# Optimization experiments

Measured on AMD Instinct MI355X. Metric: run time of the kernel, lower is better.

## Reference

```python
import jax, jax.numpy as jnp
import numpy as np

S, B, E, H, DFF = 1024, 4, 1024, 16, 4096
D = E // H  # head_dim = 64
EPS = 1e-5


def setup_inputs() -> dict:
    key = jax.random.key(0)
    ks = jax.random.split(key, 16)
    rn = lambda k, shape, s: jax.random.normal(k, shape, jnp.float32) * s
    # RoPE tables (half-rotation), theta=10000
    inv_freq = 1.0 / (10000.0 ** (jnp.arange(0, D, 2, dtype=jnp.float32) / D))  # [D/2]
    ang = jnp.arange(S, dtype=jnp.float32)[:, None] * inv_freq[None, :]          # [S, D/2]
    return {
        "q": rn(ks[0], (S, B, E), 1.0),
        "in_proj_w": rn(ks[1], (3 * E, E), E ** -0.5),
        "in_proj_b": rn(ks[2], (3 * E,), 0.02),
        "out_w": rn(ks[3], (E, E), E ** -0.5),
        "out_b": rn(ks[4], (E,), 0.02),
        "ln1_g": jnp.ones((E,), jnp.float32) + rn(ks[5], (E,), 0.02),
        "ln1_b": rn(ks[6], (E,), 0.02),
        "ln2_g": jnp.ones((E,), jnp.float32) + rn(ks[7], (E,), 0.02),
        "ln2_b": rn(ks[8], (E,), 0.02),
        "ff1_w": rn(ks[9], (DFF, E), E ** -0.5),
        "ff1_b": rn(ks[10], (DFF,), 0.02),
        "ff2_w": rn(ks[11], (E, DFF), DFF ** -0.5),
        "ff2_b": rn(ks[12], (E,), 0.02),
        "rope_cos": jnp.cos(ang),
        "rope_sin": jnp.sin(ang),
    }


def _layernorm(x, g, b):
    mu = jnp.mean(x, -1, keepdims=True)
    var = jnp.mean((x - mu) ** 2, -1, keepdims=True)
    return (x - mu) * jax.lax.rsqrt(var + EPS) * g + b


def reference(q, in_proj_w, in_proj_b, out_w, out_b, ln1_g, ln1_b, ln2_g, ln2_b,
              ff1_w, ff1_b, ff2_w, ff2_b, rope_cos, rope_sin):
    s, b, e = q.shape
    d = 2 * rope_cos.shape[-1]
    h = e // d
    # pre-norm (self-attention: k = v = q, so norm computed once)
    xq = _layernorm(q, ln1_g, ln1_b)
    # fused QKV projection
    qkv = xq @ in_proj_w.T + in_proj_b            # [s, b, 3e]
    qh, kh, vh = jnp.split(qkv, 3, axis=-1)
    qh = qh.reshape(s, b, h, d)
    kh = kh.reshape(s, b, h, d)
    vh = vh.reshape(s, b, h, d)

    def rope(t):
        t1, t2 = jnp.split(t, 2, axis=-1)          # [s, b, h, d/2] each
        c = rope_cos[:, None, None, :]
        sn = rope_sin[:, None, None, :]
        return jnp.concatenate([t1 * c - t2 * sn, t1 * sn + t2 * c], axis=-1)

    qh = rope(qh)
    kh = rope(kh)
    # attention (ssmax='none' -> identity scaling, dropout=0, no masks)
    scores = jnp.einsum("sbhd,tbhd->bhst", qh, kh) / jnp.sqrt(jnp.float32(d))
    attn = jax.nn.softmax(scores, axis=-1)
    ao = jnp.einsum("bhst,tbhd->sbhd", attn, vh).reshape(s, b, e)
    ao = ao @ out_w.T + out_b
    # residual + pre-norm FFN
    x = q + ao
    y = _layernorm(x, ln2_g, ln2_b)
    ff = jax.nn.gelu(y @ ff1_w.T + ff1_b, approximate=False) @ ff2_w.T + ff2_b
    return x + ff
```

## Files before the change

kernel.cpp:

```cpp
#include <hip/hip_runtime.h>
#include <hip/hip_bf16.h>
#include <stdint.h>

typedef float f32x4 __attribute__((ext_vector_type(4)));
typedef __bf16 bf16x8 __attribute__((ext_vector_type(8)));

__device__ __forceinline__ unsigned short f2bf(float f) {
    union { float f; unsigned u; } v; v.f = f;
    unsigned r = v.u + 0x7fffu + ((v.u >> 16) & 1u);
    return (unsigned short)(r >> 16);
}
__device__ __forceinline__ float bf2f(unsigned short u) {
    union { unsigned u; float f; } v; v.u = ((unsigned)u) << 16;
    return v.f;
}
__device__ __forceinline__ unsigned cvt_pk_bf16(float lo, float hi) {
    unsigned r;
    asm("v_cvt_pk_bf16_f32 %0, %1, %2" : "=v"(r) : "v"(lo), "v"(hi));
    return r;
}

__device__ __forceinline__ void gl_lds16(const void* g, void* l) {
    __builtin_amdgcn_global_load_lds(
        (const __attribute__((address_space(1))) void*)(unsigned long long)(uintptr_t)g,
        (__attribute__((address_space(3))) void*)(unsigned)(uintptr_t)l,
        16, 0, 0);
}

__global__ __launch_bounds__(256) void cvt_kernel(const float* __restrict__ in,
                                                  unsigned short* __restrict__ outp) {
    int i = blockIdx.x * 256 + threadIdx.x;
    float4 v = ((const float4*)in)[i];
    ushort4 o;
    o.x = f2bf(v.x); o.y = f2bf(v.y); o.z = f2bf(v.z); o.w = f2bf(v.w);
    ((ushort4*)outp)[i] = o;
}

__global__ __launch_bounds__(256) void ln_kernel(const float* __restrict__ x,
                                                 const float* __restrict__ g,
                                                 const float* __restrict__ b,
                                                 unsigned short* __restrict__ outp) {
    const int row = blockIdx.x;
    const int t = threadIdx.x;
    const float4 v = ((const float4*)(x + (size_t)row * 1024))[t];
    float s = v.x + v.y + v.z + v.w;
    float s2 = v.x * v.x + v.y * v.y + v.z * v.z + v.w * v.w;
    #pragma unroll
    for (int off = 1; off < 64; off <<= 1) {
        s  += __shfl_xor(s, off);
        s2 += __shfl_xor(s2, off);
    }
    __shared__ float red[8];
    const int w = t >> 6;
    if ((t & 63) == 0) { red[w * 2] = s; red[w * 2 + 1] = s2; }
    __syncthreads();
    s  = red[0] + red[2] + red[4] + red[6];
    s2 = red[1] + red[3] + red[5] + red[7];
    const float mu = s * (1.0f / 1024.0f);
    const float var = s2 * (1.0f / 1024.0f) - mu * mu;
    const float rstd = rsqrtf(var + 1e-5f);
    const float4 gv = ((const float4*)g)[t];
    const float4 bv = ((const float4*)b)[t];
    ushort4 o;
    o.x = f2bf((v.x - mu) * rstd * gv.x + bv.x);
    o.y = f2bf((v.y - mu) * rstd * gv.y + bv.y);
    o.z = f2bf((v.z - mu) * rstd * gv.z + bv.z);
    o.w = f2bf((v.w - mu) * rstd * gv.w + bv.w);
    ((ushort4*)(outp + (size_t)row * 1024))[t] = o;
}

__global__ __launch_bounds__(512) void rope_kernel(const unsigned short* __restrict__ qkv,
                                                   const float* __restrict__ rc,
                                                   const float* __restrict__ rs,
                                                   unsigned short* __restrict__ Qr,
                                                   unsigned short* __restrict__ Kr) {
    const int sb = blockIdx.x;
    const int s = sb >> 2, b = sb & 3;
    const int t = threadIdx.x;
    const int h = t >> 5, d = t & 31;
    const size_t rowo = (size_t)sb * 3072;
    const float c = rc[s * 32 + d];
    const float sn = rs[s * 32 + d];
    const size_t ho = ((size_t)(b * 16 + h) * 1024 + s) * 64;

    const float q1 = bf2f(qkv[rowo + h * 64 + d]);
    const float q2 = bf2f(qkv[rowo + h * 64 + d + 32]);
    Qr[ho + d]      = f2bf((q1 * c - q2 * sn) * 0.125f);
    Qr[ho + d + 32] = f2bf((q1 * sn + q2 * c) * 0.125f);

    const float k1 = bf2f(qkv[rowo + 1024 + h * 64 + d]);
    const float k2 = bf2f(qkv[rowo + 1024 + h * 64 + d + 32]);
    Kr[ho + d]      = f2bf(k1 * c - k2 * sn);
    Kr[ho + d + 32] = f2bf(k1 * sn + k2 * c);
}

__global__ __launch_bounds__(256) void vt_kernel(const unsigned short* __restrict__ qkv,
                                                 unsigned short* __restrict__ Vt) {
    __shared__ unsigned short t[64][66];
    const int s0 = blockIdx.x * 64;
    const int bh = blockIdx.y;
    const int b = bh >> 4, h = bh & 15;
    const int tid = threadIdx.x;
    const int si = tid >> 3, c = (tid & 7) * 8;
    #pragma unroll
    for (int r = 0; r < 2; r++) {
        const int s = si + r * 32;
        union { uint4 u; unsigned short sh[8]; } v;
        v.u = *(const uint4*)&qkv[((size_t)(s0 + s) * 4 + b) * 3072 + 2048 + h * 64 + c];
        #pragma unroll
        for (int i = 0; i < 8; i++) t[c + i][s] = v.sh[i];
    }
    __syncthreads();
    #pragma unroll
    for (int r = 0; r < 2; r++) {
        const int d = si + r * 32;
        const unsigned* rp = (const unsigned*)((const char*)&t[0][0] + d * 132 + c * 2);
        uint4 ov;
        ov.x = rp[0]; ov.y = rp[1]; ov.z = rp[2]; ov.w = rp[3];
        *(uint4*)&Vt[((size_t)bh * 64 + d) * 1024 + s0 + c] = ov;
    }
}

template <int EPI>
__global__ __launch_bounds__(512, 4)
void gemmW(const unsigned short* __restrict__ A, const unsigned short* __restrict__ Bw,
           const float* __restrict__ bias, unsigned short* __restrict__ Cout,
           int N, int K, int nbx) {
    __shared__ __attribute__((aligned(16))) unsigned short smem[32768];
    unsigned short* As = smem;
    unsigned short* Bs = smem + 16384;

    const int nwg = gridDim.x;
    const int swz = (blockIdx.x & 7) * (nwg >> 3) + (blockIdx.x >> 3);
    const int by = swz / nbx, bx = swz % nbx;
    const int bm = by * 256, bn = bx * 128;

    const int tid = threadIdx.x;
    const int w = tid >> 6, l = tid & 63;
    const int wr = w >> 2, wc = w & 3;
    const int lm = l & 15, lg = l >> 4, lx = lm & 7;

    const int srow = tid >> 3;
    const int sgx = ((tid & 7) ^ (srow & 7)) * 8;
    const int sdst = (tid & 7) * 8;
    const unsigned short* Ag = A + (size_t)(bm + srow) * K + sgx;
    const unsigned short* Bg = Bw + (size_t)(bn + srow) * K + sgx;

    const int c0 = ((lg ^ lx) << 3);
    const int c1 = (((4 + lg) ^ lx) << 3);

    f32x4 acc[8][2];
    #pragma unroll
    for (int i = 0; i < 8; i++)
        #pragma unroll
        for (int j = 0; j < 2; j++) acc[i][j] = f32x4{0.f, 0.f, 0.f, 0.f};

    const int arow = wr * 128 + lm;
    const int brow = wc * 32 + lm;

    for (int k0 = 0; k0 < K; k0 += 64) {
        __syncthreads();
        #pragma unroll
        for (int i = 0; i < 4; i++)
            gl_lds16(Ag + (size_t)(i * 64) * K + k0, &As[(srow + i * 64) * 64 + sdst]);
        #pragma unroll
        for (int i = 0; i < 2; i++)
            gl_lds16(Bg + (size_t)(i * 64) * K + k0, &Bs[(srow + i * 64) * 64 + sdst]);
        __syncthreads();
        #pragma unroll
        for (int h = 0; h < 2; h++) {
            const int cc = h ? c1 : c0;
            bf16x8 af[8], bfr[2];
            #pragma unroll
            for (int ni = 0; ni < 2; ni++)
                bfr[ni] = *(const bf16x8*)&Bs[(brow + ni * 16) * 64 + cc];
            #pragma unroll
            for (int mi = 0; mi < 8; mi++)
                af[mi] = *(const bf16x8*)&As[(arow + mi * 16) * 64 + cc];
            #pragma unroll
            for (int mi = 0; mi < 8; mi++)
                #pragma unroll
                for (int ni = 0; ni < 2; ni++)
                    acc[mi][ni] = __builtin_amdgcn_mfma_f32_16x16x32_bf16(
                        af[mi], bfr[ni], acc[mi][ni], 0, 0, 0);
        }
    }

    __syncthreads();
    const int r0l = wr * 128 + lg * 4;
    #pragma unroll
    for (int ni = 0; ni < 2; ni++) {
        const int col = wc * 32 + ni * 16 + lm;
        const float bc = bias[bn + col];
        #pragma unroll
        for (int mi = 0; mi < 8; mi++) {
            #pragma unroll
            for (int j = 0; j < 4; j++) {
                const int row = r0l + mi * 16 + j;
                float v = acc[mi][ni][j] + bc;
                if constexpr (EPI == 2)
                    v = 0.5f * v * (1.0f + erff(v * 0.70710678118654752f));
                smem[row * 128 + col] = f2bf(v);
            }
        }
    }
    __syncthreads();
    const int orow = tid >> 4, oseg = (tid & 15) * 8;
    #pragma unroll
    for (int p = 0; p < 8; p++) {
        const int row = p * 32 + orow;
        const uint4 v = *(const uint4*)&smem[row * 128 + oseg];
        *(uint4*)&Cout[(size_t)(bm + row) * N + bn + oseg] = v;
    }
}

template <int EPI, int BM, int BN, int WM, int WN, bool CM>
__global__ __launch_bounds__((BM / WM) * (BN / WN) * 64, 2)
void gemm4(const unsigned short* __restrict__ A, const unsigned short* __restrict__ Bw,
           const float* __restrict__ bias, const float* __restrict__ res,
           void* __restrict__ Cout, int N, int K, int nbx) {
    constexpr int WAVES_N = BN / WN;
    constexpr int THREADS = (BM / WM) * (BN / WN) * 64;
    constexpr int MR = WM / 16, NR = WN / 16;
    constexpr int ASZ = BM * 64, BSZ = BN * 64;
    constexpr int RPP = THREADS / 8;
    static_assert(BM / RPP + BN / RPP == 8, "STAGE must issue exactly 8 loads");
    __shared__ __attribute__((aligned(16))) unsigned short As[2 * ASZ];
    __shared__ __attribute__((aligned(16))) unsigned short Bs[2 * BSZ];

    const int nwg = gridDim.x;
    const int swz = (blockIdx.x & 7) * (nwg >> 3) + (blockIdx.x >> 3);
    const int nby = nwg / nbx;
    const int bx = CM ? (swz / nby) : (swz % nbx);
    const int by = CM ? (swz % nby) : (swz / nbx);
    const int bm = by * BM, bn = bx * BN;

    const int tid = threadIdx.x;
    const int w = tid >> 6, l = tid & 63;
    const int wr = w / WAVES_N, wc = w % WAVES_N;
    const int lm = l & 15, lg = l >> 4, lx = lm & 7;

    const int srow = tid >> 3;
    const int sgx = ((tid & 7) ^ (srow & 7)) * 8;
    const unsigned short* Ag = A + (size_t)(bm + srow) * K + sgx;
    const unsigned short* Bg = Bw + (size_t)(bn + srow) * K + sgx;

    const int c0 = ((lg ^ lx) << 3);
    const int c1 = (((4 + lg) ^ lx) << 3);

    f32x4 acc[MR][NR];
    #pragma unroll
    for (int i = 0; i < MR; i++)
        #pragma unroll
        for (int j = 0; j < NR; j++) acc[i][j] = f32x4{0.f, 0.f, 0.f, 0.f};

    auto STAGE = [&](int buf, int k0) {
        #pragma unroll
        for (int i = 0; i < BM / RPP; i++)
            gl_lds16(Ag + (size_t)i * RPP * K + k0, &As[buf * ASZ + i * RPP * 64 + tid * 8]);
        #pragma unroll
        for (int i = 0; i < BN / RPP; i++)
            gl_lds16(Bg + (size_t)i * RPP * K + k0, &Bs[buf * BSZ + i * RPP * 64 + tid * 8]);
    };

    const int NT = K >> 6;
    STAGE(0, 0);
    STAGE(1, 64);

    int cur = 0;
    for (int t = 0; t < NT; ++t) {
        if (t + 1 < NT) asm volatile("s_waitcnt vmcnt(8)" ::: "memory");
        else            asm volatile("s_waitcnt vmcnt(0)" ::: "memory");
        __builtin_amdgcn_s_barrier();
        asm volatile("" ::: "memory");

        const int ab = cur * ASZ, bb = cur * BSZ;
        #pragma unroll
        for (int h = 0; h < 2; h++) {
            const int cc = h ? c1 : c0;
            bf16x8 af[MR], bfr[NR];
            #pragma unroll
            for (int mi = 0; mi < MR; mi++)
                af[mi] = *(const bf16x8*)&As[ab + (wr * WM + mi * 16 + lm) * 64 + cc];
            #pragma unroll
            for (int ni = 0; ni < NR; ni++)
                bfr[ni] = *(const bf16x8*)&Bs[bb + (wc * WN + ni * 16 + lm) * 64 + cc];
            __builtin_amdgcn_s_setprio(1);
            #pragma unroll
            for (int mi = 0; mi < MR; mi++)
                #pragma unroll
                for (int ni = 0; ni < NR; ni++)
                    acc[mi][ni] = __builtin_amdgcn_mfma_f32_16x16x32_bf16(
                        af[mi], bfr[ni], acc[mi][ni], 0, 0, 0);
            __builtin_amdgcn_s_setprio(0);
        }

        asm volatile("" ::: "memory");
        __builtin_amdgcn_s_barrier();
        asm volatile("" ::: "memory");
        if (t + 2 < NT) STAGE(cur, (t + 2) << 6);
        cur ^= 1;
    }

    const int r0 = bm + wr * WM + lg * 4;
    #pragma unroll
    for (int ni = 0; ni < NR; ni++) {
        const int col = bn + wc * WN + ni * 16 + lm;
        const float bc = bias[col];
        #pragma unroll
        for (int mi = 0; mi < MR; mi++) {
            #pragma unroll
            for (int j = 0; j < 4; j++) {
                const int row = r0 + mi * 16 + j;
                const size_t idx = (size_t)row * N + col;
                const float v = acc[mi][ni][j] + bc;
                if constexpr (EPI == 0) {
                    ((unsigned short*)Cout)[idx] = f2bf(v);
                } else if constexpr (EPI == 1) {
                    ((float*)Cout)[idx] = v + res[idx];
                } else if constexpr (EPI == 2) {
                    const float ge = 0.5f * v * (1.0f + erff(v * 0.70710678118654752f));
                    ((unsigned short*)Cout)[idx] = f2bf(ge);
                } else {
                    ((float*)Cout)[idx] = v + res[idx];
                }
            }
        }
    }
}

__global__ __launch_bounds__(256, 4)
void attn_kernel(const unsigned short* __restrict__ Qr, const unsigned short* __restrict__ Kr,
                 const unsigned short* __restrict__ Vt, unsigned short* __restrict__ AO) {
    __shared__ __attribute__((aligned(16))) unsigned short Ks[64][72];
    __shared__ __attribute__((aligned(16))) unsigned short Vs[64][72];
    const int tid = threadIdx.x;
    const int w = tid >> 6, l = tid & 63;
    const int lm = l & 15, lg = l >> 4;
    const int qt = blockIdx.x, bh = blockIdx.y;
    const size_t hoff = (size_t)bh * (1024 * 64);

    const size_t qrow = hoff + (size_t)(qt * 64 + w * 16 + lm) * 64;
    const bf16x8 qf0 = *(const bf16x8*)&Qr[qrow + lg * 8];
    const bf16x8 qf1 = *(const bf16x8*)&Qr[qrow + 32 + lg * 8];

    float m = -1e30f, lsum = 0.f;
    f32x4 acc[4];
    #pragma unroll
    for (int i = 0; i < 4; i++) acc[i] = f32x4{0.f, 0.f, 0.f, 0.f};

    const int sr = tid >> 3, scc = (tid & 7) * 8;
    const int srcA = lm + 16 * ((2 * lg) & 3);
    const int srcB = lm + 16 * ((2 * lg + 1) & 3);
    const bool hi2 = (lg & 2) != 0;

    uint4 kr0 = *(const uint4*)&Kr[hoff + (size_t)sr * 64 + scc];
    uint4 kr1 = *(const uint4*)&Kr[hoff + (size_t)(sr + 32) * 64 + scc];
    uint4 vr0 = *(const uint4*)&Vt[hoff + (size_t)sr * 1024 + scc];
    uint4 vr1 = *(const uint4*)&Vt[hoff + (size_t)(sr + 32) * 1024 + scc];

    for (int kt = 0; kt < 16; kt++) {
        __syncthreads();
        *(uint4*)&Ks[sr][scc]      = kr0;
        *(uint4*)&Ks[sr + 32][scc] = kr1;
        *(uint4*)&Vs[sr][scc]      = vr0;
        *(uint4*)&Vs[sr + 32][scc] = vr1;
        __syncthreads();
        if (kt < 15) {
            const size_t kb = hoff + (size_t)(kt + 1) * 64 * 64;
            kr0 = *(const uint4*)&Kr[kb + (size_t)sr * 64 + scc];
            kr1 = *(const uint4*)&Kr[kb + (size_t)(sr + 32) * 64 + scc];
            vr0 = *(const uint4*)&Vt[hoff + (size_t)sr * 1024 + (kt + 1) * 64 + scc];
            vr1 = *(const uint4*)&Vt[hoff + (size_t)(sr + 32) * 1024 + (kt + 1) * 64 + scc];
        }

        f32x4 st[4];
        #pragma unroll
        for (int nt = 0; nt < 4; nt++) {
            const bf16x8 kf0 = *(const bf16x8*)&Ks[nt * 16 + lm][lg * 8];
            const bf16x8 kf1 = *(const bf16x8*)&Ks[nt * 16 + lm][32 + lg * 8];
            f32x4 s = f32x4{0.f, 0.f, 0.f, 0.f};
            s = __builtin_amdgcn_mfma_f32_16x16x32_bf16(kf0, qf0, s, 0, 0, 0);
            s = __builtin_amdgcn_mfma_f32_16x16x32_bf16(kf1, qf1, s, 0, 0, 0);
            st[nt] = s;
        }

        float tmax = st[0][0];
        #pragma unroll
        for (int nt = 0; nt < 4; nt++)
            #pragma unroll
            for (int j = 0; j < 4; j++) tmax = fmaxf(tmax, st[nt][j]);
        tmax = fmaxf(tmax, __shfl_xor(tmax, 16));
        tmax = fmaxf(tmax, __shfl_xor(tmax, 32));

        const float mnew = fmaxf(m, tmax);
        const float fac = __builtin_amdgcn_exp2f((m - mnew) * 1.4426950408889634f);
        m = mnew;

        unsigned pd[4][2];
        float rsum = 0.f;
        #pragma unroll
        for (int nt = 0; nt < 4; nt++) {
            const float p0 = __builtin_amdgcn_exp2f((st[nt][0] - mnew) * 1.4426950408889634f);
            const float p1 = __builtin_amdgcn_exp2f((st[nt][1] - mnew) * 1.4426950408889634f);
            const float p2 = __builtin_amdgcn_exp2f((st[nt][2] - mnew) * 1.4426950408889634f);
            const float p3 = __builtin_amdgcn_exp2f((st[nt][3] - mnew) * 1.4426950408889634f);
            rsum += (p0 + p1) + (p2 + p3);
            pd[nt][0] = cvt_pk_bf16(p0, p1);
            pd[nt][1] = cvt_pk_bf16(p2, p3);
        }
        rsum += __shfl_xor(rsum, 16);
        rsum += __shfl_xor(rsum, 32);
        lsum = lsum * fac + rsum;
        #pragma unroll
        for (int nt2 = 0; nt2 < 4; nt2++)
            #pragma unroll
            for (int j = 0; j < 4; j++) acc[nt2][j] *= fac;

        #pragma unroll
        for (int kt2 = 0; kt2 < 2; kt2++) {
            const int a0 = __shfl((int)pd[kt2 * 2][0], srcA);
            const int a1 = __shfl((int)pd[kt2 * 2 + 1][0], srcA);
            const int a2 = __shfl((int)pd[kt2 * 2][1], srcA);
            const int a3 = __shfl((int)pd[kt2 * 2 + 1][1], srcA);
            const int b0 = __shfl((int)pd[kt2 * 2][0], srcB);
            const int b1 = __shfl((int)pd[kt2 * 2 + 1][0], srcB);
            const int b2 = __shfl((int)pd[kt2 * 2][1], srcB);
            const int b3 = __shfl((int)pd[kt2 * 2 + 1][1], srcB);
            union { int u[4]; bf16x8 v; } pf;
            pf.u[0] = hi2 ? a1 : a0;
            pf.u[1] = hi2 ? a3 : a2;
            pf.u[2] = hi2 ? b1 : b0;
            pf.u[3] = hi2 ? b3 : b2;
            #pragma unroll
            for (int nt2 = 0; nt2 < 4; nt2++) {
                const bf16x8 vf = *(const bf16x8*)&Vs[nt2 * 16 + lm][kt2 * 32 + lg * 8];
                acc[nt2] = __builtin_amdgcn_mfma_f32_16x16x32_bf16(vf, pf.v, acc[nt2], 0, 0, 0);
            }
        }
    }

    const int b = bh >> 4, h = bh & 15;
    const float inv = 1.0f / lsum;
    const int s = qt * 64 + w * 16 + lm;
    #pragma unroll
    for (int nt2 = 0; nt2 < 4; nt2++) {
        ushort4 o;
        o.x = f2bf(acc[nt2][0] * inv);
        o.y = f2bf(acc[nt2][1] * inv);
        o.z = f2bf(acc[nt2][2] * inv);
        o.w = f2bf(acc[nt2][3] * inv);
        *(ushort4*)&AO[(size_t)(s * 4 + b) * 1024 + h * 64 + nt2 * 16 + lg * 4] = o;
    }
}

extern "C" void kernel_launch(void* const* d_in, const int* in_sizes, int n_in,
                              void* d_out, int out_size, void* d_ws, size_t ws_size,
                              hipStream_t stream) {
    const float* q    = (const float*)d_in[0];
    const float* w_in = (const float*)d_in[1];
    const float* b_in = (const float*)d_in[2];
    const float* w_o  = (const float*)d_in[3];
    const float* b_o  = (const float*)d_in[4];
    const float* g1   = (const float*)d_in[5];
    const float* be1  = (const float*)d_in[6];
    const float* g2   = (const float*)d_in[7];
    const float* be2  = (const float*)d_in[8];
    const float* w1   = (const float*)d_in[9];
    const float* b1   = (const float*)d_in[10];
    const float* w2   = (const float*)d_in[11];
    const float* b2   = (const float*)d_in[12];
    const float* rc   = (const float*)d_in[13];
    const float* rsn  = (const float*)d_in[14];
    float* outp = (float*)d_out;

    char* base = (char*)d_ws;
    if (ws_size < 109051904ull) return;

    unsigned short* wb_in  = (unsigned short*)(base + 0);
    unsigned short* wb_out = wb_in + 3145728;
    unsigned short* wb_ff1 = wb_out + 1048576;
    unsigned short* wb_ff2 = wb_ff1 + 4194304;
    unsigned short* xq  = (unsigned short*)(base + 25165824);
    unsigned short* qkv = (unsigned short*)(base + 33554432);
    unsigned short* hh  = (unsigned short*)(base + 33554432);
    unsigned short* Qr  = (unsigned short*)(base + 58720256);
    unsigned short* Kr  = (unsigned short*)(base + 67108864);
    unsigned short* Vt  = (unsigned short*)(base + 75497472);
    unsigned short* ao  = (unsigned short*)(base + 83886080);
    float*          x   = (float*)(base + 92274688);
    unsigned short* y   = xq;

    cvt_kernel<<<3072, 256, 0, stream>>>(w_in, wb_in);
    cvt_kernel<<<1024, 256, 0, stream>>>(w_o, wb_out);
    cvt_kernel<<<4096, 256, 0, stream>>>(w1, wb_ff1);
    cvt_kernel<<<4096, 256, 0, stream>>>(w2, wb_ff2);

    ln_kernel<<<4096, 256, 0, stream>>>(q, g1, be1, xq);
    gemmW<0><<<384, 512, 0, stream>>>(xq, wb_in, b_in, qkv, 3072, 1024, 24);
    rope_kernel<<<4096, 512, 0, stream>>>(qkv, rc, rsn, Qr, Kr);
    vt_kernel<<<dim3(16, 64), 256, 0, stream>>>(qkv, Vt);
    attn_kernel<<<dim3(16, 64), 256, 0, stream>>>(Qr, Kr, Vt, ao);
    gemm4<1, 128, 128, 64, 64, true><<<256, 256, 0, stream>>>(ao, wb_out, b_o, q, x, 1024, 1024, 8);
    ln_kernel<<<4096, 256, 0, stream>>>(x, g2, be2, y);
    gemmW<2><<<512, 512, 0, stream>>>(y, wb_ff1, b1, hh, 4096, 1024, 32);
    gemm4<3, 128, 128, 64, 64, true><<<256, 256, 0, stream>>>(hh, wb_ff2, b2, x, outp, 1024, 4096, 8);
}
```

Measured before the change: 226.5 us.

## Group GEMM tile rasterization for L2 reuse and widen attention KV tiles

Adds a grouped tile-mapping helper so consecutive workgroups on each XCD cover a compact GR×GC block of output tiles. This improves L2 reuse of the A and B panels in the QKV, out-proj and FFN GEMMs, and gemm4 is specialised to a fixed 128x128 shape. The attention kernel now processes 128 keys per iteration instead of 64, halving the loop trips and barriers. The cost is more registers for scores and prefetch buffers, plus larger LDS, which may reduce occupancy.

```diff
diff --git a/kernel.cpp b/kernel.cpp
--- a/kernel.cpp
+++ b/kernel.cpp
@@ -25,6 +25,16 @@
         (const __attribute__((address_space(1))) void*)(unsigned long long)(uintptr_t)g,
         (__attribute__((address_space(3))) void*)(unsigned)(uintptr_t)l,
         16, 0, 0);
+}
+
+__device__ __forceinline__ void tile_map(int bid, int nwg, int nbx, int GR, int GC,
+                                         int* bx, int* by) {
+    const int swz = (bid & 7) * (nwg >> 3) + (bid >> 3);
+    const int CH = nwg >> 3;
+    const int chunk = swz / CH, ii = swz % CH;
+    const int KC = nbx / GC;
+    *bx = (chunk % KC) * GC + (ii % GC);
+    *by = (chunk / KC) * GR + (ii / GC);
 }
 
 __global__ __launch_bounds__(256) void cvt_kernel(const float* __restrict__ in,
@@ -121,7 +131,7 @@
     }
 }
 
-template <int EPI>
+template <int EPI, int GR, int GC>
 __global__ __launch_bounds__(512, 4)
 void gemmW(const unsigned short* __restrict__ A, const unsigned short* __restrict__ Bw,
            const float* __restrict__ bias, unsigned short* __restrict__ Cout,
@@ -130,9 +140,8 @@
     unsigned short* As = smem;
     unsigned short* Bs = smem + 16384;
 
-    const int nwg = gridDim.x;
-    const int swz = (blockIdx.x & 7) * (nwg >> 3) + (blockIdx.x >> 3);
-    const int by = swz / nbx, bx = swz % nbx;
+    int bx, by;
+    tile_map(blockIdx.x, gridDim.x, nbx, GR, GC, &bx, &by);
     const int bm = by * 256, bn = bx * 128;
 
     const int tid = threadIdx.x;
@@ -214,30 +223,22 @@
     }
 }
 
-template <int EPI, int BM, int BN, int WM, int WN, bool CM>
-__global__ __launch_bounds__((BM / WM) * (BN / WN) * 64, 2)
+template <int EPI, int GR, int GC>
+__global__ __launch_bounds__(256, 2)
 void gemm4(const unsigned short* __restrict__ A, const unsigned short* __restrict__ Bw,
            const float* __restrict__ bias, const float* __restrict__ res,
            void* __restrict__ Cout, int N, int K, int nbx) {
-    constexpr int WAVES_N = BN / WN;
-    constexpr int THREADS = (BM / WM) * (BN / WN) * 64;
-    constexpr int MR = WM / 16, NR = WN / 16;
-    constexpr int ASZ = BM * 64, BSZ = BN * 64;
-    constexpr int RPP = THREADS / 8;
-    static_assert(BM / RPP + BN / RPP == 8, "STAGE must issue exactly 8 loads");
+    constexpr int ASZ = 128 * 64, BSZ = 128 * 64;
     __shared__ __attribute__((aligned(16))) unsigned short As[2 * ASZ];
     __shared__ __attribute__((aligned(16))) unsigned short Bs[2 * BSZ];
 
-    const int nwg = gridDim.x;
-    const int swz = (blockIdx.x & 7) * (nwg >> 3) + (blockIdx.x >> 3);
-    const int nby = nwg / nbx;
-    const int bx = CM ? (swz / nby) : (swz % nbx);
-    const int by = CM ? (swz % nby) : (swz / nbx);
-    const int bm = by * BM, bn = bx * BN;
+    int bx, by;
+    tile_map(blockIdx.x, gridDim.x, nbx, GR, GC, &bx, &by);
+    const int bm = by * 128, bn = bx * 128;
 
     const int tid = threadIdx.x;
     const int w = tid >> 6, l = tid & 63;
-    const int wr = w / WAVES_N, wc = w % WAVES_N;
+    const int wr = w >> 1, wc = w & 1;
     const int lm = l & 15, lg = l >> 4, lx = lm & 7;
 
     const int srow = tid >> 3;
@@ -248,19 +249,19 @@
     const int c0 = ((lg ^ lx) << 3);
     const int c1 = (((4 + lg) ^ lx) << 3);
 
-    f32x4 acc[MR][NR];
-    #pragma unroll
-    for (int i = 0; i < MR; i++)
-        #pragma unroll
-        for (int j = 0; j < NR; j++) acc[i][j] = f32x4{0.f, 0.f, 0.f, 0.f};
+    f32x4 acc[4][4];
+    #pragma unroll
+    for (int i = 0; i < 4; i++)
+        #pragma unroll
+        for (int j = 0; j < 4; j++) acc[i][j] = f32x4{0.f, 0.f, 0.f, 0.f};
 
     auto STAGE = [&](int buf, int k0) {
         #pragma unroll
-        for (int i = 0; i < BM / RPP; i++)
-            gl_lds16(Ag + (size_t)i * RPP * K + k0, &As[buf * ASZ + i * RPP * 64 + tid * 8]);
-        #pragma unroll
-        for (int i = 0; i < BN / RPP; i++)
-            gl_lds16(Bg + (size_t)i * RPP * K + k0, &Bs[buf * BSZ + i * RPP * 64 + tid * 8]);
+        for (int i = 0; i < 4; i++)
+            gl_lds16(Ag + (size_t)i * 32 * K + k0, &As[buf * ASZ + i * 32 * 64 + tid * 8]);
+        #pragma unroll
+        for (int i = 0; i < 4; i++)
+            gl_lds16(Bg + (size_t)i * 32 * K + k0, &Bs[buf * BSZ + i * 32 * 64 + tid * 8]);
     };
 
     const int NT = K >> 6;
@@ -278,18 +279,18 @@
         #pragma unroll
         for (int h = 0; h < 2; h++) {
             const int cc = h ? c1 : c0;
-            bf16x8 af[MR], bfr[NR];
-            #pragma unroll
-            for (int mi = 0; mi < MR; mi++)
-                af[mi] = *(const bf16x8*)&As[ab + (wr * WM + mi * 16 + lm) * 64 + cc];
-            #pragma unroll
-            for (int ni = 0; ni < NR; ni++)
-                bfr[ni] = *(const bf16x8*)&Bs[bb + (wc * WN + ni * 16 + lm) * 64 + cc];
+            bf16x8 af[4], bfr[4];
+            #pragma unroll
+            for (int mi = 0; mi < 4; mi++)
+                af[mi] = *(const bf16x8*)&As[ab + (wr * 64 + mi * 16 + lm) * 64 + cc];
+            #pragma unroll
+            for (int ni = 0; ni < 4; ni++)
+                bfr[ni] = *(const bf16x8*)&Bs[bb + (wc * 64 + ni * 16 + lm) * 64 + cc];
             __builtin_amdgcn_s_setprio(1);
             #pragma unroll
-            for (int mi = 0; mi < MR; mi++)
+            for (int mi = 0; mi < 4; mi++)
                 #pragma unroll
-                for (int ni = 0; ni < NR; ni++)
+                for (int ni = 0; ni < 4; ni++)
                     acc[mi][ni] = __builtin_amdgcn_mfma_f32_16x16x32_bf16(
                         af[mi], bfr[ni], acc[mi][ni], 0, 0, 0);
             __builtin_amdgcn_s_setprio(0);
@@ -302,13 +303,13 @@
         cur ^= 1;
     }
 
-    const int r0 = bm + wr * WM + lg * 4;
-    #pragma unroll
-    for (int ni = 0; ni < NR; ni++) {
-        const int col = bn + wc * WN + ni * 16 + lm;
+    const int r0 = bm + wr * 64 + lg * 4;
+    #pragma unroll
+    for (int ni = 0; ni < 4; ni++) {
+        const int col = bn + wc * 64 + ni * 16 + lm;
         const float bc = bias[col];
         #pragma unroll
-        for (int mi = 0; mi < MR; mi++) {
+        for (int mi = 0; mi < 4; mi++) {
             #pragma unroll
             for (int j = 0; j < 4; j++) {
                 const int row = r0 + mi * 16 + j;
@@ -316,8 +317,6 @@
                 const float v = acc[mi][ni][j] + bc;
                 if constexpr (EPI == 0) {
                     ((unsigned short*)Cout)[idx] = f2bf(v);
-                } else if constexpr (EPI == 1) {
-                    ((float*)Cout)[idx] = v + res[idx];
                 } else if constexpr (EPI == 2) {
                     const float ge = 0.5f * v * (1.0f + erff(v * 0.70710678118654752f));
                     ((unsigned short*)Cout)[idx] = f2bf(ge);
@@ -332,8 +331,8 @@
 __global__ __launch_bounds__(256, 4)
 void attn_kernel(const unsigned short* __restrict__ Qr, const unsigned short* __restrict__ Kr,
                  const unsigned short* __restrict__ Vt, unsigned short* __restrict__ AO) {
-    __shared__ __attribute__((aligned(16))) unsigned short Ks[64][72];
-    __shared__ __attribute__((aligned(16))) unsigned short Vs[64][72];
+    __shared__ __attribute__((aligned(16))) unsigned short Ks[128][72];
+    __shared__ __attribute__((aligned(16))) unsigned short Vs[64][136];
     const int tid = threadIdx.x;
     const int w = tid >> 6, l = tid & 63;
     const int lm = l & 15, lg = l >> 4;
@@ -349,34 +348,39 @@
     #pragma unroll
     for (int i = 0; i < 4; i++) acc[i] = f32x4{0.f, 0.f, 0.f, 0.f};
 
-    const int sr = tid >> 3, scc = (tid & 7) * 8;
+    const int ksr = tid >> 3, kscc = (tid & 7) * 8;
+    const int vsr = tid >> 4, vscc = (tid & 15) * 8;
     const int srcA = lm + 16 * ((2 * lg) & 3);
     const int srcB = lm + 16 * ((2 * lg + 1) & 3);
     const bool hi2 = (lg & 2) != 0;
 
-    uint4 kr0 = *(const uint4*)&Kr[hoff + (size_t)sr * 64 + scc];
-    uint4 kr1 = *(const uint4*)&Kr[hoff + (size_t)(sr + 32) * 64 + scc];
-    uint4 vr0 = *(const uint4*)&Vt[hoff + (size_t)sr * 1024 + scc];
-    uint4 vr1 = *(const uint4*)&Vt[hoff + (size_t)(sr + 32) * 1024 + scc];
-
-    for (int kt = 0; kt < 16; kt++) {
+    uint4 kr[4], vr[4];
+    #pragma unroll
+    for (int r = 0; r < 4; r++) {
+        kr[r] = *(const uint4*)&Kr[hoff + (size_t)(ksr + r * 32) * 64 + kscc];
+        vr[r] = *(const uint4*)&Vt[hoff + (size_t)(vsr + r * 16) * 1024 + vscc];
+    }
+
+    for (int kt = 0; kt < 8; kt++) {
         __syncthreads();
-        *(uint4*)&Ks[sr][scc]      = kr0;
-        *(uint4*)&Ks[sr + 32][scc] = kr1;
-        *(uint4*)&Vs[sr][scc]      = vr0;
-        *(uint4*)&Vs[sr + 32][scc] = vr1;
+        #pragma unroll
+        for (int r = 0; r < 4; r++) {
+            *(uint4*)&Ks[ksr + r * 32][kscc] = kr[r];
+            *(uint4*)&Vs[vsr + r * 16][vscc] = vr[r];
+        }
         __syncthreads();
-        if (kt < 15) {
-            const size_t kb = hoff + (size_t)(kt + 1) * 64 * 64;
-            kr0 = *(const uint4*)&Kr[kb + (size_t)sr * 64 + scc];
-            kr1 = *(const uint4*)&Kr[kb + (size_t)(sr + 32) * 64 + scc];
-            vr0 = *(const uint4*)&Vt[hoff + (size_t)sr * 1024 + (kt + 1) * 64 + scc];
-            vr1 = *(const uint4*)&Vt[hoff + (size_t)(sr + 32) * 1024 + (kt + 1) * 64 + scc];
-        }
-
-        f32x4 st[4];
-        #pragma unroll
-        for (int nt = 0; nt < 4; nt++) {
+        if (kt < 7) {
+            const size_t kb = hoff + (size_t)(kt + 1) * 128 * 64;
+            #pragma unroll
+            for (int r = 0; r < 4; r++) {
+                kr[r] = *(const uint4*)&Kr[kb + (size_t)(ksr + r * 32) * 64 + kscc];
+                vr[r] = *(const uint4*)&Vt[hoff + (size_t)(vsr + r * 16) * 1024 + (kt + 1) * 128 + vscc];
+            }
+        }
+
+        f32x4 st[8];
+        #pragma unroll
+        for (int nt = 0; nt < 8; nt++) {
             const bf16x8 kf0 = *(const bf16x8*)&Ks[nt * 16 + lm][lg * 8];
             const bf16x8 kf1 = *(const bf16x8*)&Ks[nt * 16 + lm][32 + lg * 8];
             f32x4 s = f32x4{0.f, 0.f, 0.f, 0.f};
@@ -387,7 +391,7 @@
 
         float tmax = st[0][0];
         #pragma unroll
-        for (int nt = 0; nt < 4; nt++)
+        for (int nt = 0; nt < 8; nt++)
             #pragma unroll
             for (int j = 0; j < 4; j++) tmax = fmaxf(tmax, st[nt][j]);
         tmax = fmaxf(tmax, __shfl_xor(tmax, 16));
@@ -397,10 +401,10 @@
         const float fac = __builtin_amdgcn_exp2f((m - mnew) * 1.4426950408889634f);
         m = mnew;
 
-        unsigned pd[4][2];
+        unsigned pd[8][2];
         float rsum = 0.f;
         #pragma unroll
-        for (int nt = 0; nt < 4; nt++) {
+        for (int nt = 0; nt < 8; nt++) {
             const float p0 = __builtin_amdgcn_exp2f((st[nt][0] - mnew) * 1.4426950408889634f);
             const float p1 = __builtin_amdgcn_exp2f((st[nt][1] - mnew) * 1.4426950408889634f);
             const float p2 = __builtin_amdgcn_exp2f((st[nt][2] - mnew) * 1.4426950408889634f);
@@ -418,7 +422,7 @@
             for (int j = 0; j < 4; j++) acc[nt2][j] *= fac;
 
         #pragma unroll
-        for (int kt2 = 0; kt2 < 2; kt2++) {
+        for (int kt2 = 0; kt2 < 4; kt2++) {
             const int a0 = __shfl((int)pd[kt2 * 2][0], srcA);
             const int a1 = __shfl((int)pd[kt2 * 2 + 1][0], srcA);
             const int a2 = __shfl((int)pd[kt2 * 2][1], srcA);
@@ -497,12 +501,12 @@
     cvt_kernel<<<4096, 256, 0, stream>>>(w2, wb_ff2);
 
     ln_kernel<<<4096, 256, 0, stream>>>(q, g1, be1, xq);
-    gemmW<0><<<384, 512, 0, stream>>>(xq, wb_in, b_in, qkv, 3072, 1024, 24);
+    gemmW<0, 8, 6><<<384, 512, 0, stream>>>(xq, wb_in, b_in, qkv, 3072, 1024, 24);
     rope_kernel<<<4096, 512, 0, stream>>>(qkv, rc, rsn, Qr, Kr);
     vt_kernel<<<dim3(16, 64), 256, 0, stream>>>(qkv, Vt);
     attn_kernel<<<dim3(16, 64), 256, 0, stream>>>(Qr, Kr, Vt, ao);
-    gemm4<1, 128, 128, 64, 64, true><<<256, 256, 0, stream>>>(ao, wb_out, b_o, q, x, 1024, 1024, 8);
+    gemm4<1, 8, 4><<<256, 256, 0, stream>>>(ao, wb_out, b_o, q, x, 1024, 1024, 8);
     ln_kernel<<<4096, 256, 0, stream>>>(x, g2, be2, y);
-    gemmW<2><<<512, 512, 0, stream>>>(y, wb_ff1, b1, hh, 4096, 1024, 32);
-    gemm4<3, 128, 128, 64, 64, true><<<256, 256, 0, stream>>>(hh, wb_ff2, b2, x, outp, 1024, 4096, 8);
-}
+    gemmW<2, 8, 8><<<512, 512, 0, stream>>>(y, wb_ff1, b1, hh, 4096, 1024, 32);
+    gemm4<3, 8, 4><<<256, 256, 0, stream>>>(hh, wb_ff2, b2, x, outp, 1024, 4096, 8);
+}
```

New measurement: 286.3 us. +26.4%, slower.
